# Optimization experiments

Measured on AMD Instinct MI355X. Metric: run time of the kernel, lower is better.

## Reference

```python
import jax, jax.numpy as jnp
import numpy as np

B, S, L, C, H, D, CP = 32, 4, 64, 32, 4, 8, 16  # batch, tracks, bins, c_msa, heads, d_head, c_pair


def _ln(x, g, b, eps=1e-5):
    m = jnp.mean(x, axis=-1, keepdims=True)
    v = jnp.mean((x - m) ** 2, axis=-1, keepdims=True)
    return (x - m) / jnp.sqrt(v + eps) * g + b


def setup_inputs() -> dict:
    key = jax.random.key(0)
    ks = jax.random.split(key, 20)
    n = lambda k, shape, s=0.1: jax.random.normal(k, shape, jnp.float32) * s
    return dict(
        chip_ctcf=n(ks[0], (B, L), 1.0),
        chip_hac=n(ks[1], (B, L), 1.0),
        chip_me1=n(ks[2], (B, L), 1.0),
        chip_me3=n(ks[3], (B, L), 1.0),
        bulk_map=n(ks[4], (B, 1, L, L), 1.0),
        we_w=n(ks[5], (C, 1)), we_b=jnp.zeros((C,), jnp.float32),
        pos=n(ks[6], (1, 1, L, C)),
        mn_g=jnp.ones((C,), jnp.float32), mn_b=jnp.zeros((C,), jnp.float32),
        wq=n(ks[7], (C, C)), bq=jnp.zeros((C,), jnp.float32),
        wk=n(ks[8], (C, C)), bk=jnp.zeros((C,), jnp.float32),
        wv=n(ks[9], (C, C)), bv=jnp.zeros((C,), jnp.float32),
        wo=n(ks[10], (C, C)), bo=jnp.zeros((C,), jnp.float32),
        an_g=jnp.ones((C,), jnp.float32), an_b=jnp.zeros((C,), jnp.float32),
        conv_w=n(ks[11], (H,)), conv_b=jnp.zeros((H,), jnp.float32),
        gate_w=n(ks[12], (H, D, D)), gate_b=jnp.zeros((H, D), jnp.float32),
        pp_w=n(ks[13], (CP, C * C), 0.03), pp_b=jnp.zeros((CP,), jnp.float32),
        ada_g=jnp.ones((CP,), jnp.float32), ada_b=jnp.zeros((CP,), jnp.float32),
        ada_alpha=jnp.ones((1,), jnp.float32),
    )


def reference(chip_ctcf, chip_hac, chip_me1, chip_me3, bulk_map,
              we_w, we_b, pos, mn_g, mn_b,
              wq, bq, wk, bk, wv, bv, wo, bo, an_g, an_b,
              conv_w, conv_b, gate_w, gate_b,
              pp_w, pp_b, ada_g, ada_b, ada_alpha):
    # 1) build MSA: (B, S=4, L, C)
    signals = jnp.stack([chip_ctcf, chip_hac, chip_me1, chip_me3], axis=1)  # (B,S,L)
    msa = signals[..., None] * we_w[:, 0] + we_b                            # Linear(1,C)
    x = _ln(msa + pos, mn_g, mn_b)                                          # (B,S,L,C)

    # 2) row self-attention with bulk-derived per-head bias
    q = (x @ wq.T + bq).reshape(B, S, L, H, D)
    k = (x @ wk.T + bk).reshape(B, S, L, H, D)
    v = (x @ wv.T + bv).reshape(B, S, L, H, D)
    scores = jnp.einsum('bslhd,bsmhd->bshlm', q, k) / jnp.sqrt(jnp.float32(D))
    bias = bulk_map * conv_w.reshape(1, H, 1, 1) + conv_b.reshape(1, H, 1, 1)  # 1x1 conv -> (B,H,L,L)
    attn = jax.nn.softmax(scores + bias[:, None], axis=-1)                     # (B,S,H,L,L)
    out = jnp.einsum('bshlm,bsmhd->bshld', attn, v)
    gate = jax.nn.sigmoid(jnp.einsum('hcd,bshld->bshlc', gate_w, out)
                          + gate_b[None, None, :, None, :])
    out = out * gate
    out = out.transpose(0, 1, 3, 2, 4).reshape(B, S, L, C)
    out = out @ wo.T + bo
    x = _ln(x + out, an_g, an_b)                                            # post-attn LayerNorm

    # 3) outer-product (of max over tracks) pair features
    m = jnp.max(x, axis=1)                                                  # (B,L,C)
    pair = jnp.einsum('bic,bjd->bijcd', m, m).reshape(B, L, L, C * C)       # (B,L,L,1024)
    nrm = jnp.sqrt(jnp.sum(pair * pair, axis=-1, keepdims=True))
    pair = pair / jnp.maximum(nrm, 1e-6)                                    # F.normalize
    feat = pair @ pp_w.T + pp_b                                             # (B,L,L,CP)
    feat = feat + ada_alpha * _ln(feat, ada_g, ada_b)                       # AdaNorm
    feat = jax.nn.silu(feat)
    return feat.transpose(0, 3, 1, 2)                                       # (B,CP,L,L)
```

## Files before the change

### kernel.cpp

```cpp
#include <hip/hip_runtime.h>
#include <hip/hip_bf16.h>

#define NB 32
#define NS 4
#define NL 64
#define NC 32
#define NH 4
#define ND 8
#define NCP 16

using fp = const float* __restrict__;

__global__ __launch_bounds__(256) void k1_attn(
    fp ctcf, fp hac, fp me1, fp me3, fp bulk,
    fp we_w, fp we_b, fp pos, fp mn_g, fp mn_b,
    fp wq, fp bq, fp wk, fp bk, fp wv, fp bv,
    fp wo, fp bo, fp an_g, fp an_b,
    fp conv_w, fp conv_b, fp gate_w, fp gate_b,
    float* __restrict__ xpostT)
{
    __shared__ float qs_s[NC*NL];
    __shared__ float ks_s[NC*NL];
    __shared__ float vs_s[NC*NL];
    __shared__ float xs_s[NC*NL];
    __shared__ float ao_s[NC*NL];
    __shared__ float bulk_s[32*65];
    __shared__ float red1[32*8], red2[32*8];
    __shared__ float mstat[32], istat[32];

    const int t    = threadIdx.x;
    const int w    = t >> 6;
    const int l    = t & 63;
    const int bx   = blockIdx.x;
    const int b    = bx >> 3;
    const int s    = (bx >> 1) & 3;
    const int half = bx & 1;

    for (int idx = t; idx < 32*NL; idx += 256){
        int lr = idx >> 6, m = idx & 63;
        bulk_s[lr*65 + m] = bulk[b*NL*NL + (half*32 + lr)*NL + m];
    }

    fp sigp = (s == 0) ? ctcf : (s == 1) ? hac : (s == 2) ? me1 : me3;
    const float sig = sigp[b*NL + l];

    float x[NC];
    float mean = 0.f;
#pragma unroll
    for (int c = 0; c < NC; c++){
        x[c] = sig * we_w[c] + we_b[c] + pos[l*NC + c];
        mean += x[c];
    }
    mean *= (1.f/NC);
    float var = 0.f;
#pragma unroll
    for (int c = 0; c < NC; c++){ float d = x[c] - mean; var += d*d; }
    var *= (1.f/NC);
    float inv = rsqrtf(var + 1e-5f);
#pragma unroll
    for (int c = 0; c < NC; c++) x[c] = (x[c] - mean)*inv*mn_g[c] + mn_b[c];

#pragma unroll
    for (int e8 = 0; e8 < ND; e8++){
        int e = w*ND + e8;
        float aq = bq[e], ak = bk[e], av = bv[e];
#pragma unroll
        for (int c = 0; c < NC; c++){
            float xv = x[c];
            aq += xv * wq[e*NC + c];
            ak += xv * wk[e*NC + c];
            av += xv * wv[e*NC + c];
        }
        qs_s[e*NL + l] = aq;
        ks_s[e*NL + l] = ak;
        vs_s[e*NL + l] = av;
        xs_s[e*NL + l] = x[e];
    }
    __syncthreads();

    const int rl  = l >> 1;
    const int r   = half*32 + rl;
    const int mh_ = l & 1;
    const int m0  = mh_*32;

    float q8[ND];
#pragma unroll
    for (int d = 0; d < ND; d++) q8[d] = qs_s[(w*ND + d)*NL + r];

    const float rs8 = 0.35355339059327373f;
    const float cw = conv_w[w], cb = conv_b[w];
    float srow[32];
    float mx = -1e30f;
    for (int mi = 0; mi < 32; mi++){
        int m = m0 + mi;
        float dot = 0.f;
#pragma unroll
        for (int d = 0; d < ND; d++)
            dot += q8[d] * ks_s[(w*ND + d)*NL + m];
        float v = dot*rs8 + bulk_s[rl*65 + m]*cw + cb;
        srow[mi] = v;
        mx = fmaxf(mx, v);
    }
    mx = fmaxf(mx, __shfl_xor(mx, 1));
    float sm = 0.f;
    for (int mi = 0; mi < 32; mi++){ srow[mi] = __expf(srow[mi] - mx); sm += srow[mi]; }
    sm += __shfl_xor(sm, 1);
    float is = 1.f / sm;

    float o[ND];
#pragma unroll
    for (int d = 0; d < ND; d++) o[d] = 0.f;
    for (int mi = 0; mi < 32; mi++){
        float a = srow[mi] * is;
#pragma unroll
        for (int d = 0; d < ND; d++)
            o[d] += a * vs_s[(w*ND + d)*NL + m0 + mi];
    }
#pragma unroll
    for (int d = 0; d < ND; d++) o[d] += __shfl_xor(o[d], 1);

#pragma unroll
    for (int k = 0; k < 4; k++){
        int c8 = mh_*4 + k;
        float g = gate_b[w*ND + c8];
#pragma unroll
        for (int d = 0; d < ND; d++) g += gate_w[(w*ND + c8)*ND + d] * o[d];
        ao_s[(w*ND + c8)*NL + r] = o[c8] * (1.f/(1.f + __expf(-g)));
    }
    __syncthreads();

    const int r3  = t & 31;
    const int rg  = half*32 + r3;
    const int cg  = t >> 5;
    float vals[4];
    float psum = 0.f, psq = 0.f;
#pragma unroll
    for (int k = 0; k < 4; k++){
        int c = cg*4 + k;
        float a = bo[c];
#pragma unroll
        for (int e = 0; e < NC; e++) a += ao_s[e*NL + rg] * wo[c*NC + e];
        float val = xs_s[c*NL + rg] + a;
        vals[k] = val; psum += val; psq += val*val;
    }
    red1[r3*8 + cg] = psum;
    red2[r3*8 + cg] = psq;
    __syncthreads();
    if (t < 32){
        float sum = 0.f, ssq = 0.f;
#pragma unroll
        for (int g = 0; g < 8; g++){ sum += red1[t*8 + g]; ssq += red2[t*8 + g]; }
        float mn = sum * (1.f/NC);
        float vr = ssq * (1.f/NC) - mn*mn;
        mstat[t] = mn;
        istat[t] = rsqrtf(vr + 1e-5f);
    }
    __syncthreads();
    {
        float mn = mstat[r3], iv = istat[r3];
#pragma unroll
        for (int k = 0; k < 4; k++){
            int c = cg*4 + k;
            xpostT[((b*NS + s)*NC + c)*NL + rg] = (vals[k] - mn)*iv*an_g[c] + an_b[c];
        }
    }
}

__global__ __launch_bounds__(256) void k23_pair(
    const float* __restrict__ xpostT, fp pp_w,
    fp pp_b, fp ada_g, fp ada_b, fp ada_alpha,
    float* __restrict__ out)
{
    __shared__ float ppws[8*NC*NC];
    __shared__ float mh[NC*NL];
    __shared__ float u[NCP*4*NC];

    const int b  = blockIdx.x >> 4;
    const int it = blockIdx.x & 15;
    const int t  = threadIdx.x;
    const int w  = t >> 6;
    const int j  = t & 63;

    const float* xb = xpostT + b*NS*NC*NL;
#pragma unroll
    for (int k = 0; k < 8; k++){
        int cj = k*256 + t;
        float v = xb[cj];
        v = fmaxf(v, xb[NC*NL + cj]);
        v = fmaxf(v, xb[2*NC*NL + cj]);
        v = fmaxf(v, xb[3*NC*NL + cj]);
        mh[cj] = v;
    }
    __syncthreads();

    if (t < NL){
        float sq = 0.f;
#pragma unroll
        for (int c = 0; c < NC; c++){ float v = mh[c*NL + t]; sq += v*v; }
        u[t] = 1.f / fmaxf(sqrtf(sq), 1e-3f);
    }
    {
        const float4* src = (const float4*)(pp_w);
        float4* dst = (float4*)ppws;
#pragma unroll
        for (int k = 0; k < 8; k++) dst[k*256 + t] = src[k*256 + t];
    }
    __syncthreads();

#pragma unroll
    for (int k = 0; k < 8; k++){
        int cj = k*256 + t;
        mh[cj] *= u[cj & 63];
    }
    __syncthreads();

    float md[NC];
#pragma unroll
    for (int c = 0; c < NC; c++) md[c] = mh[c*NL + j];

#pragma unroll
    for (int loop = 0; loop < 4; loop++){
        int idx = loop*256 + t;
        int d  = idx & 31;
        int ip = (idx >> 5) & 3;
        int pl = idx >> 7;
        int i  = it*4 + ip;
        float acc = 0.f;
#pragma unroll
        for (int c = 0; c < NC; c++)
            acc += mh[c*NL + i] * ppws[pl*1024 + c*32 + d];
        u[pl*128 + ip*32 + d] = acc;
    }
    __syncthreads();

    {
        const float4* src = (const float4*)(pp_w + 8*NC*NC);
        float4* dst = (float4*)ppws;
#pragma unroll
        for (int k = 0; k < 8; k++) dst[k*256 + t] = src[k*256 + t];
    }
    __syncthreads();

#pragma unroll
    for (int loop = 0; loop < 4; loop++){
        int idx = loop*256 + t;
        int d  = idx & 31;
        int ip = (idx >> 5) & 3;
        int pl = idx >> 7;
        int i  = it*4 + ip;
        float acc = 0.f;
#pragma unroll
        for (int c = 0; c < NC; c++)
            acc += mh[c*NL + i] * ppws[pl*1024 + c*32 + d];
        u[(8 + pl)*128 + ip*32 + d] = acc;
    }
    __syncthreads();

    float f[NCP];
#pragma unroll 1
    for (int p = 0; p < NCP; p++){
        float a = 0.f;
#pragma unroll
        for (int d = 0; d < NC; d++)
            a += u[p*128 + w*32 + d] * md[d];
        f[p] = a;
    }

    const float alpha = ada_alpha[0];
    float fsum = 0.f, fsq = 0.f;
#pragma unroll
    for (int p = 0; p < NCP; p++){
        float v = f[p] + pp_b[p];
        f[p] = v; fsum += v; fsq += v*v;
    }
    float fmean = fsum * (1.f/NCP);
    float fvar  = fsq * (1.f/NCP) - fmean*fmean;
    float finv  = rsqrtf(fvar + 1e-5f);
    const int i = it*4 + w;
#pragma unroll
    for (int p = 0; p < NCP; p++){
        float v = f[p] + alpha * ((f[p] - fmean)*finv*ada_g[p] + ada_b[p]);
        out[((b*NCP + p)*NL + i)*NL + j] = v / (1.f + __expf(-v));
    }
}

extern "C" void kernel_launch(void* const* d_in, const int* in_sizes, int n_in,
                              void* d_out, int out_size, void* d_ws, size_t ws_size,
                              hipStream_t stream)
{
    float* xpostT = (float*)d_ws;

    k1_attn<<<NB*NS*2, 256, 0, stream>>>(
        (fp)d_in[0], (fp)d_in[1], (fp)d_in[2], (fp)d_in[3], (fp)d_in[4],
        (fp)d_in[5], (fp)d_in[6], (fp)d_in[7], (fp)d_in[8], (fp)d_in[9],
        (fp)d_in[10], (fp)d_in[11], (fp)d_in[12], (fp)d_in[13], (fp)d_in[14], (fp)d_in[15],
        (fp)d_in[16], (fp)d_in[17], (fp)d_in[18], (fp)d_in[19],
        (fp)d_in[20], (fp)d_in[21], (fp)d_in[22], (fp)d_in[23], xpostT);

    k23_pair<<<NB*16, 256, 0, stream>>>(
        xpostT, (fp)d_in[24], (fp)d_in[25], (fp)d_in[26], (fp)d_in[27], (fp)d_in[28],
        (float*)d_out);
}
```

Before: 142.7 us.

## Double attention block threads and split each query row across four lanes

The attention kernel now launches 512 threads per block instead of 256. Each query row is split across four lanes of 16 keys each rather than two lanes of 32, and the softmax and output reductions use an extra shuffle step. The score loops are fully unrolled, so the smaller 16-entry score array can stay in registers instead of being indexed dynamically and possibly spilling to scratch. The QKV projection and output-projection work is re-partitioned to match, at the cost of some redundant gating computation and a larger LayerNorm reduction.

```diff
diff --git a/kernel.cpp b/kernel.cpp
--- a/kernel.cpp
+++ b/kernel.cpp
@@ -11,7 +11,7 @@
 
 using fp = const float* __restrict__;
 
-__global__ __launch_bounds__(256) void k1_attn(
+__global__ __launch_bounds__(512) void k1_attn(
     fp ctcf, fp hac, fp me1, fp me3, fp bulk,
     fp we_w, fp we_b, fp pos, fp mn_g, fp mn_b,
     fp wq, fp bq, fp wk, fp bk, fp wv, fp bv,
@@ -25,7 +25,7 @@
     __shared__ float xs_s[NC*NL];
     __shared__ float ao_s[NC*NL];
     __shared__ float bulk_s[32*65];
-    __shared__ float red1[32*8], red2[32*8];
+    __shared__ float red1[32*17], red2[32*17];
     __shared__ float mstat[32], istat[32];
 
     const int t    = threadIdx.x;
@@ -36,7 +36,7 @@
     const int s    = (bx >> 1) & 3;
     const int half = bx & 1;
 
-    for (int idx = t; idx < 32*NL; idx += 256){
+    for (int idx = t; idx < 32*NL; idx += 512){
         int lr = idx >> 6, m = idx & 63;
         bulk_s[lr*65 + m] = bulk[b*NL*NL + (half*32 + lr)*NL + m];
     }
@@ -61,8 +61,12 @@
     for (int c = 0; c < NC; c++) x[c] = (x[c] - mean)*inv*mn_g[c] + mn_b[c];
 
 #pragma unroll
-    for (int e8 = 0; e8 < ND; e8++){
-        int e = w*ND + e8;
+    for (int c = 0; c < NC; c++)
+        if ((c >> 2) == w) xs_s[c*NL + l] = x[c];
+
+#pragma unroll
+    for (int e4 = 0; e4 < 4; e4++){
+        int e = w*4 + e4;
         float aq = bq[e], ak = bk[e], av = bv[e];
 #pragma unroll
         for (int c = 0; c < NC; c++){
@@ -74,82 +78,91 @@
         qs_s[e*NL + l] = aq;
         ks_s[e*NL + l] = ak;
         vs_s[e*NL + l] = av;
-        xs_s[e*NL + l] = x[e];
-    }
-    __syncthreads();
-
-    const int rl  = l >> 1;
+    }
+    __syncthreads();
+
+    const int h   = w >> 1;
+    const int sub = ((w & 1) << 6) | l;
+    const int rl  = sub >> 2;
+    const int q4  = sub & 3;
     const int r   = half*32 + rl;
-    const int mh_ = l & 1;
-    const int m0  = mh_*32;
+    const int m0  = q4*16;
 
     float q8[ND];
 #pragma unroll
-    for (int d = 0; d < ND; d++) q8[d] = qs_s[(w*ND + d)*NL + r];
+    for (int d = 0; d < ND; d++) q8[d] = qs_s[(h*ND + d)*NL + r];
 
     const float rs8 = 0.35355339059327373f;
-    const float cw = conv_w[w], cb = conv_b[w];
-    float srow[32];
+    const float cw = conv_w[h], cb = conv_b[h];
+    float srow[16];
     float mx = -1e30f;
-    for (int mi = 0; mi < 32; mi++){
+#pragma unroll
+    for (int mi = 0; mi < 16; mi++){
         int m = m0 + mi;
         float dot = 0.f;
 #pragma unroll
         for (int d = 0; d < ND; d++)
-            dot += q8[d] * ks_s[(w*ND + d)*NL + m];
+            dot += q8[d] * ks_s[(h*ND + d)*NL + m];
         float v = dot*rs8 + bulk_s[rl*65 + m]*cw + cb;
         srow[mi] = v;
         mx = fmaxf(mx, v);
     }
     mx = fmaxf(mx, __shfl_xor(mx, 1));
+    mx = fmaxf(mx, __shfl_xor(mx, 2));
     float sm = 0.f;
-    for (int mi = 0; mi < 32; mi++){ srow[mi] = __expf(srow[mi] - mx); sm += srow[mi]; }
+#pragma unroll
+    for (int mi = 0; mi < 16; mi++){ srow[mi] = __expf(srow[mi] - mx); sm += srow[mi]; }
     sm += __shfl_xor(sm, 1);
+    sm += __shfl_xor(sm, 2);
     float is = 1.f / sm;
 
     float o[ND];
 #pragma unroll
     for (int d = 0; d < ND; d++) o[d] = 0.f;
-    for (int mi = 0; mi < 32; mi++){
+#pragma unroll
+    for (int mi = 0; mi < 16; mi++){
         float a = srow[mi] * is;
 #pragma unroll
         for (int d = 0; d < ND; d++)
-            o[d] += a * vs_s[(w*ND + d)*NL + m0 + mi];
-    }
-#pragma unroll
-    for (int d = 0; d < ND; d++) o[d] += __shfl_xor(o[d], 1);
-
-#pragma unroll
-    for (int k = 0; k < 4; k++){
-        int c8 = mh_*4 + k;
-        float g = gate_b[w*ND + c8];
-#pragma unroll
-        for (int d = 0; d < ND; d++) g += gate_w[(w*ND + c8)*ND + d] * o[d];
-        ao_s[(w*ND + c8)*NL + r] = o[c8] * (1.f/(1.f + __expf(-g)));
+            o[d] += a * vs_s[(h*ND + d)*NL + m0 + mi];
+    }
+#pragma unroll
+    for (int d = 0; d < ND; d++){
+        o[d] += __shfl_xor(o[d], 1);
+        o[d] += __shfl_xor(o[d], 2);
+    }
+
+#pragma unroll
+    for (int c8 = 0; c8 < ND; c8++){
+        float g = gate_b[h*ND + c8];
+#pragma unroll
+        for (int d = 0; d < ND; d++) g += gate_w[(h*ND + c8)*ND + d] * o[d];
+        float val = o[c8] * (1.f/(1.f + __expf(-g)));
+        if ((c8 >> 1) == q4) ao_s[(h*ND + c8)*NL + r] = val;
     }
     __syncthreads();
 
     const int r3  = t & 31;
     const int rg  = half*32 + r3;
     const int cg  = t >> 5;
-    float vals[4];
+    float vals[2];
     float psum = 0.f, psq = 0.f;
 #pragma unroll
-    for (int k = 0; k < 4; k++){
-        int c = cg*4 + k;
+    for (int k = 0; k < 2; k++){
+        int c = cg*2 + k;
         float a = bo[c];
 #pragma unroll
         for (int e = 0; e < NC; e++) a += ao_s[e*NL + rg] * wo[c*NC + e];
         float val = xs_s[c*NL + rg] + a;
         vals[k] = val; psum += val; psq += val*val;
     }
-    red1[r3*8 + cg] = psum;
-    red2[r3*8 + cg] = psq;
+    red1[r3*17 + cg] = psum;
+    red2[r3*17 + cg] = psq;
     __syncthreads();
     if (t < 32){
         float sum = 0.f, ssq = 0.f;
 #pragma unroll
-        for (int g = 0; g < 8; g++){ sum += red1[t*8 + g]; ssq += red2[t*8 + g]; }
+        for (int g = 0; g < 16; g++){ sum += red1[t*17 + g]; ssq += red2[t*17 + g]; }
         float mn = sum * (1.f/NC);
         float vr = ssq * (1.f/NC) - mn*mn;
         mstat[t] = mn;
@@ -159,8 +172,8 @@
     {
         float mn = mstat[r3], iv = istat[r3];
 #pragma unroll
-        for (int k = 0; k < 4; k++){
-            int c = cg*4 + k;
+        for (int k = 0; k < 2; k++){
+            int c = cg*2 + k;
             xpostT[((b*NS + s)*NC + c)*NL + rg] = (vals[k] - mn)*iv*an_g[c] + an_b[c];
         }
     }
@@ -290,7 +303,7 @@
 {
     float* xpostT = (float*)d_ws;
 
-    k1_attn<<<NB*NS*2, 256, 0, stream>>>(
+    k1_attn<<<NB*NS*2, 512, 0, stream>>>(
         (fp)d_in[0], (fp)d_in[1], (fp)d_in[2], (fp)d_in[3], (fp)d_in[4],
         (fp)d_in[5], (fp)d_in[6], (fp)d_in[7], (fp)d_in[8], (fp)d_in[9],
         (fp)d_in[10], (fp)d_in[11], (fp)d_in[12], (fp)d_in[13], (fp)d_in[14], (fp)d_in[15],
```

Result: no change. 143.1 us (+0.3%).
